# Optimization experiments

Hardware: AMD Instinct MI355X
Metric: run time of the kernel (lower is better)

The kernel has to match this reference:

```python
import jax, jax.numpy as jnp
import numpy as np

B, S, D = 1024, 200, 512
D_FF = 256


def setup_inputs() -> dict:
    key = jax.random.key(0)
    ks = jax.random.split(key, 8)
    s = 0.02  # init scale to keep gates in a sane range
    return {
        "target": jax.random.normal(ks[0], (B, D), jnp.float32),
        "history": jax.random.normal(ks[1], (B, S, D), jnp.float32),
        "W_ih": jax.random.normal(ks[2], (3 * D, D), jnp.float32) * s,
        "W_hh": jax.random.normal(ks[3], (3 * D, D), jnp.float32) * s,
        "b_ih": jnp.zeros((3 * D,), jnp.float32),
        "b_hh": jnp.zeros((3 * D,), jnp.float32),
        "W_fc": jax.random.normal(ks[4], (D_FF, 2 * D), jnp.float32) * s,
        "b_fc": jnp.zeros((D_FF,), jnp.float32),
        "W_sc": jax.random.normal(ks[5], (1, D_FF), jnp.float32) * s,
        "b_sc": jnp.zeros((1,), jnp.float32),
    }


def _gru(history, W_ih, W_hh, b_ih, b_hh):
    # Precompute input-side gate pre-activations for all steps: [B, S, 3D]
    gx = jnp.einsum("bsd,gd->bsg", history, W_ih) + b_ih
    d = history.shape[-1]
    h0 = jnp.zeros((history.shape[0], d), history.dtype)

    def step(h, gx_t):
        gh = h @ W_hh.T + b_hh  # [B, 3D]
        xr, xz, xn = jnp.split(gx_t, 3, axis=-1)
        hr, hz, hn = jnp.split(gh, 3, axis=-1)
        r = jax.nn.sigmoid(xr + hr)
        z = jax.nn.sigmoid(xz + hz)
        n = jnp.tanh(xn + r * hn)
        h_new = (1.0 - z) * n + z * h
        return h_new, h_new

    _, out = jax.lax.scan(step, h0, jnp.swapaxes(gx, 0, 1))  # out: [S, B, D]
    return jnp.swapaxes(out, 0, 1)  # [B, S, D]


def reference(target, history, W_ih, W_hh, b_ih, b_hh, W_fc, b_fc, W_sc, b_sc):
    d = target.shape[-1]
    gru_out = _gru(history, W_ih, W_hh, b_ih, b_hh)  # [B, S, D]

    # concat([gru_out, target]) @ W_fc.T  == gru_out @ Wg.T + target @ Wt.T
    Wg, Wt = W_fc[:, :d], W_fc[:, d:]
    pre = jnp.einsum("bsd,fd->bsf", gru_out, Wg) + (target @ Wt.T)[:, None, :] + b_fc
    hidden = jax.nn.gelu(pre, approximate=False)  # torch F.gelu default is exact erf
    scores = jnp.einsum("bsf,f->bs", hidden, W_sc[0]) + b_sc[0]  # [B, S]
    w = jax.nn.softmax(scores, axis=-1)
    interest = jnp.einsum("bs,bsd->bd", w, gru_out)  # [B, D]
    return jnp.concatenate([interest, target], axis=-1)  # [B, 2D]
```

## Files before the change

kernel.cpp:

```cpp
#include <hip/hip_runtime.h>

typedef __attribute__((ext_vector_type(8))) short short8v;
typedef __attribute__((ext_vector_type(4))) float f32x4;

#define NB 1024
#define NS 200
#define ND 512
#define NG 1536
#define NM 204800
#define NFF 256

#define GRU_P 4
#define GRU_G 64

__device__ __forceinline__ float bf2f(unsigned short u){
  union { unsigned u; float f; } v; v.u = ((unsigned)u) << 16; return v.f;
}
__device__ __forceinline__ unsigned short f2bf(float f){
  union { float f; unsigned u; } v; v.f = f;
  unsigned r = v.u + 0x7fffu + ((v.u >> 16) & 1u);
  return (unsigned short)(r >> 16);
}
__device__ __forceinline__ float sigm(float x){ return 1.f / (1.f + __expf(-x)); }
__device__ __forceinline__ float tanhfast(float x){ return 1.f - 2.f / (1.f + __expf(2.f * x)); }

__global__ void k_prepack(const float* __restrict__ W, unsigned short* __restrict__ out,
                          int ld, int coloff, int ntiles){
  int gid = blockIdx.x * 256 + threadIdx.x;
  if (gid >= ntiles * 1024) return;
  int ntile = gid >> 10; int rem = gid & 1023;
  int kk = rem >> 6; int lane = rem & 63;
  int c = ntile * 16 + (lane & 15);
  int k0 = kk * 32 + (lane >> 4) * 8;
  const float* s = W + (size_t)c * ld + coloff + k0;
  uint4 v;
  v.x = (unsigned)f2bf(s[0]) | ((unsigned)f2bf(s[1]) << 16);
  v.y = (unsigned)f2bf(s[2]) | ((unsigned)f2bf(s[3]) << 16);
  v.z = (unsigned)f2bf(s[4]) | ((unsigned)f2bf(s[5]) << 16);
  v.w = (unsigned)f2bf(s[6]) | ((unsigned)f2bf(s[7]) << 16);
  *(uint4*)(out + (size_t)gid * 8) = v;
}

__global__ void k_tvec(const float* __restrict__ target, const float* __restrict__ Wfc,
                       const float* __restrict__ bfc, float* __restrict__ tvec){
  __shared__ float tg[4][ND];
  int bb = blockIdx.x;
  int tid = threadIdx.x;
  for (int idx = tid; idx < 4 * ND; idx += 256){
    int j = idx >> 9, d = idx & 511;
    tg[j][d] = target[(size_t)(bb * 4 + j) * ND + d];
  }
  __syncthreads();
  const float* wrow = Wfc + (size_t)tid * 1024 + 512;
  float a0 = 0, a1 = 0, a2 = 0, a3 = 0;
  for (int d = 0; d < ND; ++d){
    float wv = wrow[d];
    a0 += tg[0][d] * wv; a1 += tg[1][d] * wv; a2 += tg[2][d] * wv; a3 += tg[3][d] * wv;
  }
  float bias = bfc[tid];
  tvec[(size_t)(bb * 4 + 0) * NFF + tid] = a0 + bias;
  tvec[(size_t)(bb * 4 + 1) * NFF + tid] = a1 + bias;
  tvec[(size_t)(bb * 4 + 2) * NFF + tid] = a2 + bias;
  tvec[(size_t)(bb * 4 + 3) * NFF + tid] = a3 + bias;
}

__global__ __launch_bounds__(256) void k_gemm_gx(const float* __restrict__ Af,
                                                 const unsigned short* __restrict__ Bpk,
                                                 const float* __restrict__ bih,
                                                 unsigned short* __restrict__ gx){
  __shared__ unsigned short As[128 * 64];
  int tid = threadIdx.x; int lane = tid & 63; int wid = tid >> 6;
  int wm = wid >> 1, wn = wid & 1;
  int Nb = blockIdx.x, Mb = blockIdx.y;
  const float* Abase = Af + (size_t)Mb * 128 * ND;
  const short8v* Bp = (const short8v*)Bpk;
  f32x4 acc[4][4];
  #pragma unroll
  for (int i = 0; i < 4; ++i)
    #pragma unroll
    for (int j = 0; j < 4; ++j) acc[i][j] = (f32x4){0.f, 0.f, 0.f, 0.f};

  for (int kc = 0; kc < 8; ++kc){
    __syncthreads();
    #pragma unroll
    for (int pass = 0; pass < 4; ++pass){
      int idx = pass * 256 + tid; int r = idx >> 3, ch = idx & 7;
      const float* src = Abase + (size_t)r * ND + kc * 64 + ch * 8;
      float4 f0 = *(const float4*)src;
      float4 f1 = *(const float4*)(src + 4);
      uint4 v;
      v.x = (unsigned)f2bf(f0.x) | ((unsigned)f2bf(f0.y) << 16);
      v.y = (unsigned)f2bf(f0.z) | ((unsigned)f2bf(f0.w) << 16);
      v.z = (unsigned)f2bf(f1.x) | ((unsigned)f2bf(f1.y) << 16);
      v.w = (unsigned)f2bf(f1.z) | ((unsigned)f2bf(f1.w) << 16);
      *(uint4*)&As[r * 64 + ch * 8] = v;
    }
    __syncthreads();
    #pragma unroll
    for (int i = 0; i < 2; ++i){
      short8v a[4];
      #pragma unroll
      for (int mt = 0; mt < 4; ++mt)
        a[mt] = *(const short8v*)&As[(wm * 64 + mt * 16 + (lane & 15)) * 64 + i * 32 + (lane >> 4) * 8];
      #pragma unroll
      for (int nt = 0; nt < 4; ++nt){
        short8v b = Bp[((size_t)(Nb * 8 + wn * 4 + nt) * 16 + (kc * 2 + i)) * 64 + lane];
        #pragma unroll
        for (int mt = 0; mt < 4; ++mt)
          acc[mt][nt] = __builtin_amdgcn_mfma_f32_16x16x32_bf16(a[mt], b, acc[mt][nt], 0, 0, 0);
      }
    }
  }
  #pragma unroll
  for (int mt = 0; mt < 4; ++mt){
    #pragma unroll
    for (int nt = 0; nt < 4; ++nt){
      int gcol = Nb * 128 + wn * 64 + nt * 16 + (lane & 15);
      float bv = bih[gcol];
      #pragma unroll
      for (int r = 0; r < 4; ++r){
        int grow = Mb * 128 + wm * 64 + mt * 16 + (lane >> 4) * 4 + r;
        gx[(size_t)grow * NG + gcol] = f2bf(acc[mt][nt][r] + bv);
      }
    }
  }
}

__global__ __launch_bounds__(512, 1) void k_gru7(const unsigned short* __restrict__ gx,
                                                 const unsigned short* __restrict__ Wpk,
                                                 const float* __restrict__ bhh,
                                                 unsigned short* __restrict__ gout,
                                                 unsigned long long* __restrict__ hx,
                                                 int* __restrict__ flags){
  __shared__ unsigned short hbuf[2][16 * 512];
  __shared__ unsigned short hstg[16][136];
  int tid = threadIdx.x; int lane = tid & 63; int nh = tid >> 6;
  int bid = blockIdx.x; int g = bid & 63; int s = bid >> 6;
  int colg = lane & 15;
  int rowg = lane >> 4;
  int c_h = s * 128 + nh * 16 + colg;
  int b0 = g * 16;
  int* gfl = flags + g * 32;

  for (int i = tid; i < 16 * 512; i += 512) hbuf[0][i] = 0;

  short8v wf[3][16];
  const short8v* Wp = (const short8v*)Wpk;
  #pragma unroll
  for (int gg = 0; gg < 3; ++gg){
    int ntile = gg * 32 + s * 8 + nh;
    #pragma unroll
    for (int kk = 0; kk < 16; ++kk)
      wf[gg][kk] = Wp[((size_t)ntile * 16 + kk) * 64 + lane];
  }
  float bR = bhh[c_h], bZ = bhh[512 + c_h], bN = bhh[1024 + c_h];
  float hreg[4] = {0.f, 0.f, 0.f, 0.f};

  int wbat = tid >> 5;
  int wc4  = tid & 31;

  unsigned short cxr[4], cxz[4], cxn[4];
  #pragma unroll
  for (int r = 0; r < 4; ++r){
    const unsigned short* gp = gx + ((size_t)(b0 + rowg * 4 + r) * NS + 0) * NG;
    cxr[r] = gp[c_h]; cxz[r] = gp[512 + c_h]; cxn[r] = gp[1024 + c_h];
  }
  __syncthreads();

  #pragma unroll 1
  for (int t = 0; t < NS; ++t){
    int par = t & 1;
    const unsigned short* hr = hbuf[par];
    f32x4 acc0 = (f32x4){0.f,0.f,0.f,0.f}, acc1 = acc0, acc2 = acc0;
    #pragma unroll
    for (int kc = 0; kc < 16; ++kc){
      short8v a = *(const short8v*)&hr[kc * 512 + lane * 8];
      acc0 = __builtin_amdgcn_mfma_f32_16x16x32_bf16(a, wf[0][kc], acc0, 0, 0, 0);
      acc1 = __builtin_amdgcn_mfma_f32_16x16x32_bf16(a, wf[1][kc], acc1, 0, 0, 0);
      acc2 = __builtin_amdgcn_mfma_f32_16x16x32_bf16(a, wf[2][kc], acc2, 0, 0, 0);
    }
    unsigned short hnew[4];
    #pragma unroll
    for (int r = 0; r < 4; ++r){
      float rr = sigm(bf2f(cxr[r]) + acc0[r] + bR);
      float zz = sigm(bf2f(cxz[r]) + acc1[r] + bZ);
      float nn = tanhfast(bf2f(cxn[r]) + rr * (acc2[r] + bN));
      float h = nn + zz * (hreg[r] - nn);
      hreg[r] = h;
      hnew[r] = f2bf(h);
    }

    if (t + 1 < NS){
      unsigned long long* hxp = hx + (size_t)par * (1024 * 128);
      #pragma unroll
      for (int r = 0; r < 4; ++r) hstg[rowg * 4 + r][nh * 16 + colg] = hnew[r];
      __syncthreads();
      {
        unsigned long long v8 = *(const unsigned long long*)&hstg[wbat][wc4 * 4];
        __hip_atomic_store(&hxp[(size_t)(b0 + wbat) * 128 + s * 32 + wc4], v8,
                           __ATOMIC_RELAXED, __HIP_MEMORY_SCOPE_AGENT);
      }
      asm volatile("s_waitcnt vmcnt(0)" ::: "memory");
      if (lane == 0)
        __hip_atomic_store(&gfl[s * 8 + nh], t + 1, __ATOMIC_RELAXED, __HIP_MEMORY_SCOPE_AGENT);
      #pragma unroll
      for (int r = 0; r < 4; ++r)
        gout[((size_t)(b0 + rowg * 4 + r) * NS + t) * ND + c_h] = hnew[r];
      #pragma unroll
      for (int r = 0; r < 4; ++r){
        const unsigned short* gp = gx + ((size_t)(b0 + rowg * 4 + r) * NS + (t + 1)) * NG;
        cxr[r] = gp[c_h]; cxz[r] = gp[512 + c_h]; cxn[r] = gp[1024 + c_h];
      }
      {
        int need = t + 1; int fv;
        do {
          fv = (lane < 32) ? __hip_atomic_load(&gfl[lane], __ATOMIC_RELAXED, __HIP_MEMORY_SCOPE_AGENT) : need;
        } while (!__all(fv >= need));
      }
      unsigned short* hw = hbuf[par ^ 1];
      #pragma unroll
      for (int q = 0; q < 2; ++q){
        int kc = q * 8 + nh;
        size_t base = (size_t)(b0 + (lane & 15)) * 128 + kc * 8 + (lane >> 4) * 2;
        unsigned long long u0 = __hip_atomic_load(&hxp[base],     __ATOMIC_RELAXED, __HIP_MEMORY_SCOPE_AGENT);
        unsigned long long u1 = __hip_atomic_load(&hxp[base + 1], __ATOMIC_RELAXED, __HIP_MEMORY_SCOPE_AGENT);
        unsigned long long tmp[2] = {u0, u1};
        *(uint4*)&hw[kc * 512 + lane * 8] = *(const uint4*)tmp;
      }
      __syncthreads();
    } else {
      #pragma unroll
      for (int r = 0; r < 4; ++r)
        gout[((size_t)(b0 + rowg * 4 + r) * NS + t) * ND + c_h] = hnew[r];
    }
  }
}

__global__ __launch_bounds__(512) void k_gemm_s4(const unsigned short* __restrict__ A,
                                                 const unsigned short* __restrict__ Bpk,
                                                 const float* __restrict__ tvec,
                                                 const float* __restrict__ Wsc,
                                                 const float* __restrict__ bsc,
                                                 float* __restrict__ scores){
  __shared__ unsigned short As[128 * 64];
  __shared__ float spart[4][128];
  int tid = threadIdx.x; int lane = tid & 63; int wid = tid >> 6;
  int wm = wid >> 2, wn = wid & 3;
  int Mb = blockIdx.x;
  const unsigned short* Abase = A + (size_t)Mb * 128 * ND;
  const short8v* Bp = (const short8v*)Bpk;
  f32x4 acc[4][4];
  #pragma unroll
  for (int i = 0; i < 4; ++i)
    #pragma unroll
    for (int j = 0; j < 4; ++j) acc[i][j] = (f32x4){0.f, 0.f, 0.f, 0.f};

  for (int kc = 0; kc < 8; ++kc){
    __syncthreads();
    #pragma unroll
    for (int pass = 0; pass < 2; ++pass){
      int idx = pass * 512 + tid; int r = idx >> 3, ch = idx & 7;
      uint4 v = *(const uint4*)(Abase + (size_t)r * ND + kc * 64 + ch * 8);
      *(uint4*)&As[r * 64 + ch * 8] = v;
    }
    __syncthreads();
    #pragma unroll
    for (int i = 0; i < 2; ++i){
      short8v a[4];
      #pragma unroll
      for (int mt = 0; mt < 4; ++mt)
        a[mt] = *(const short8v*)&As[(wm * 64 + mt * 16 + (lane & 15)) * 64 + i * 32 + (lane >> 4) * 8];
      #pragma unroll
      for (int nt = 0; nt < 4; ++nt){
        short8v b = Bp[((size_t)(wn * 4 + nt) * 16 + (kc * 2 + i)) * 64 + lane];
        #pragma unroll
        for (int mt = 0; mt < 4; ++mt)
          acc[mt][nt] = __builtin_amdgcn_mfma_f32_16x16x32_bf16(a[mt], b, acc[mt][nt], 0, 0, 0);
      }
    }
  }
  #pragma unroll
  for (int mt = 0; mt < 4; ++mt){
    #pragma unroll
    for (int r = 0; r < 4; ++r){
      int rowl = wm * 64 + mt * 16 + (lane >> 4) * 4 + r;
      unsigned grow = (unsigned)(Mb * 128 + rowl);
      unsigned bidx = grow / 200u;
      float rowsum = 0.f;
      #pragma unroll
      for (int nt = 0; nt < 4; ++nt){
        int gcol = wn * 64 + nt * 16 + (lane & 15);
        float pre = acc[mt][nt][r] + tvec[(size_t)bidx * NFF + gcol];
        float g = 0.5f * pre * (1.f + erff(pre * 0.70710678118654752f));
        rowsum += g * Wsc[gcol];
      }
      rowsum += __shfl_xor(rowsum, 1, 64);
      rowsum += __shfl_xor(rowsum, 2, 64);
      rowsum += __shfl_xor(rowsum, 4, 64);
      rowsum += __shfl_xor(rowsum, 8, 64);
      if ((lane & 15) == 0) spart[wn][rowl] = rowsum;
    }
  }
  __syncthreads();
  if (tid < 128){
    float s = spart[0][tid] + spart[1][tid] + spart[2][tid] + spart[3][tid] + bsc[0];
    scores[(size_t)Mb * 128 + tid] = s;
  }
}

__global__ void k_out(const float* __restrict__ scores, const unsigned short* __restrict__ gout,
                      const float* __restrict__ target, float* __restrict__ out){
  int b = blockIdx.x; int tid = threadIdx.x;
  __shared__ float sw[NS];
  __shared__ float red[4];
  float v = (tid < NS) ? scores[(size_t)b * NS + tid] : -3.0e38f;
  float m = v;
  #pragma unroll
  for (int off = 32; off >= 1; off >>= 1) m = fmaxf(m, __shfl_xor(m, off, 64));
  if ((tid & 63) == 0) red[tid >> 6] = m;
  __syncthreads();
  m = fmaxf(fmaxf(red[0], red[1]), fmaxf(red[2], red[3]));
  float e = (tid < NS) ? __expf(v - m) : 0.f;
  if (tid < NS) sw[tid] = e;
  float su = e;
  #pragma unroll
  for (int off = 32; off >= 1; off >>= 1) su += __shfl_xor(su, off, 64);
  __syncthreads();
  if ((tid & 63) == 0) red[tid >> 6] = su;
  __syncthreads();
  float inv = 1.f / (red[0] + red[1] + red[2] + red[3]);
  int d0 = tid * 2;
  float a0 = 0.f, a1 = 0.f;
  const unsigned short* gbase = gout + (size_t)b * NS * ND + d0;
  for (int s = 0; s < NS; ++s){
    unsigned u = *(const unsigned*)(gbase + (size_t)s * ND);
    float wgt = sw[s];
    a0 += wgt * bf2f((unsigned short)(u & 0xffffu));
    a1 += wgt * bf2f((unsigned short)(u >> 16));
  }
  out[(size_t)b * 1024 + d0] = a0 * inv;
  out[(size_t)b * 1024 + d0 + 1] = a1 * inv;
  float2 tv = *(const float2*)(target + (size_t)b * ND + d0);
  out[(size_t)b * 1024 + 512 + d0] = tv.x;
  out[(size_t)b * 1024 + 512 + d0 + 1] = tv.y;
}

extern "C" void kernel_launch(void* const* d_in, const int* in_sizes, int n_in,
                              void* d_out, int out_size, void* d_ws, size_t ws_size,
                              hipStream_t stream) {
  const float* target  = (const float*)d_in[0];
  const float* history = (const float*)d_in[1];
  const float* W_ih    = (const float*)d_in[2];
  const float* W_hh    = (const float*)d_in[3];
  const float* b_ih    = (const float*)d_in[4];
  const float* b_hh    = (const float*)d_in[5];
  const float* W_fc    = (const float*)d_in[6];
  const float* b_fc    = (const float*)d_in[7];
  const float* W_sc    = (const float*)d_in[8];
  const float* b_sc    = (const float*)d_in[9];

  char* ws = (char*)d_ws;
  size_t off = 0;
  unsigned short* gx     = (unsigned short*)(ws + off); off += 629145600ull;
  unsigned short* gout   = (unsigned short*)(ws + off); off += 209715200ull;
  unsigned short* wih_pk = (unsigned short*)(ws + off); off += 1572864ull;
  unsigned short* whh_pk = (unsigned short*)(ws + off); off += 1572864ull;
  unsigned short* wg_pk  = (unsigned short*)(ws + off); off += 262144ull;
  float*          tvec   = (float*)(ws + off);          off += 1048576ull;
  float*          scores = (float*)(ws + off);          off += 819200ull;
  unsigned long long* hx = (unsigned long long*)(ws + off); off += 2097152ull;
  int*            flags  = (int*)(ws + off);             off += 8192ull;
  if (ws_size < off) return;
  float* outp = (float*)d_out;

  (void)hipMemsetAsync(flags, 0, GRU_G * 32 * sizeof(int), stream);
  k_prepack<<<384, 256, 0, stream>>>(W_ih, wih_pk, 512, 0, 96);
  k_prepack<<<384, 256, 0, stream>>>(W_hh, whh_pk, 512, 0, 96);
  k_prepack<<<64, 256, 0, stream>>>(W_fc, wg_pk, 1024, 0, 16);
  k_tvec<<<256, 256, 0, stream>>>(target, W_fc, b_fc, tvec);
  k_gemm_gx<<<dim3(12, 1600), 256, 0, stream>>>(history, wih_pk, b_ih, gx);
  k_gru7<<<256, 512, 0, stream>>>(gx, whh_pk, b_hh, gout, hx, flags);
  k_gemm_s4<<<1600, 512, 0, stream>>>(gout, wg_pk, tvec, W_sc, b_sc, scores);
  k_out<<<1024, 256, 0, stream>>>(scores, gout, target, outp);
}
```

Baseline: 2.041 ms.

## Narrow GRU step sync to per-wave flag pairs and fold r/z hidden bias

The GRU recurrent kernel replaces the block-wide barrier before publishing h with a wave-local LDS wait, since each wave now publishes only its own staged columns. Instead of every wave polling all 32 producer flags, each wave polls two 64-bit flag pairs covering only the k-chunks it consumes, and loads each half as soon as its producers are ready. The r/z parts of b_hh are folded into the gx GEMM bias epilogue, removing two adds per element per step. This cuts the serial per-timestep synchronization latency, but the correctness of the finer-grained dependency tracking is more delicate.

```diff
diff --git a/kernel.cpp b/kernel.cpp
--- a/kernel.cpp
+++ b/kernel.cpp
@@ -67,6 +67,7 @@
 __global__ __launch_bounds__(256) void k_gemm_gx(const float* __restrict__ Af,
                                                  const unsigned short* __restrict__ Bpk,
                                                  const float* __restrict__ bih,
+                                                 const float* __restrict__ bhh,
                                                  unsigned short* __restrict__ gx){
   __shared__ unsigned short As[128 * 64];
   int tid = threadIdx.x; int lane = tid & 63; int wid = tid >> 6;
@@ -116,7 +117,7 @@
     #pragma unroll
     for (int nt = 0; nt < 4; ++nt){
       int gcol = Nb * 128 + wn * 64 + nt * 16 + (lane & 15);
-      float bv = bih[gcol];
+      float bv = bih[gcol] + (gcol < 1024 ? bhh[gcol] : 0.f);
       #pragma unroll
       for (int r = 0; r < 4; ++r){
         int grow = Mb * 128 + wm * 64 + mt * 16 + (lane >> 4) * 4 + r;
@@ -126,7 +127,7 @@
   }
 }
 
-__global__ __launch_bounds__(512, 1) void k_gru7(const unsigned short* __restrict__ gx,
+__global__ __launch_bounds__(512, 1) void k_gru9(const unsigned short* __restrict__ gx,
                                                  const unsigned short* __restrict__ Wpk,
                                                  const float* __restrict__ bhh,
                                                  unsigned short* __restrict__ gout,
@@ -153,11 +154,12 @@
     for (int kk = 0; kk < 16; ++kk)
       wf[gg][kk] = Wp[((size_t)ntile * 16 + kk) * 64 + lane];
   }
-  float bR = bhh[c_h], bZ = bhh[512 + c_h], bN = bhh[1024 + c_h];
+  float bN = bhh[1024 + c_h];
   float hreg[4] = {0.f, 0.f, 0.f, 0.f};
 
-  int wbat = tid >> 5;
-  int wc4  = tid & 31;
+  int wpair = (nh & 3) * 2;
+  const unsigned long long* f1 = (const unsigned long long*)&gfl[(nh >> 2) * 8 + wpair];
+  const unsigned long long* f2 = (const unsigned long long*)&gfl[((nh >> 2) + 2) * 8 + wpair];
 
   unsigned short cxr[4], cxz[4], cxn[4];
   #pragma unroll
@@ -182,8 +184,8 @@
     unsigned short hnew[4];
     #pragma unroll
     for (int r = 0; r < 4; ++r){
-      float rr = sigm(bf2f(cxr[r]) + acc0[r] + bR);
-      float zz = sigm(bf2f(cxz[r]) + acc1[r] + bZ);
+      float rr = sigm(bf2f(cxr[r]) + acc0[r]);
+      float zz = sigm(bf2f(cxz[r]) + acc1[r]);
       float nn = tanhfast(bf2f(cxn[r]) + rr * (acc2[r] + bN));
       float h = nn + zz * (hreg[r] - nn);
       hreg[r] = h;
@@ -194,10 +196,10 @@
       unsigned long long* hxp = hx + (size_t)par * (1024 * 128);
       #pragma unroll
       for (int r = 0; r < 4; ++r) hstg[rowg * 4 + r][nh * 16 + colg] = hnew[r];
-      __syncthreads();
+      asm volatile("s_waitcnt lgkmcnt(0)" ::: "memory");
       {
-        unsigned long long v8 = *(const unsigned long long*)&hstg[wbat][wc4 * 4];
-        __hip_atomic_store(&hxp[(size_t)(b0 + wbat) * 128 + s * 32 + wc4], v8,
+        unsigned long long v8 = *(const unsigned long long*)&hstg[lane & 15][nh * 16 + (lane >> 4) * 4];
+        __hip_atomic_store(&hxp[(size_t)(b0 + (lane & 15)) * 128 + s * 32 + nh * 4 + (lane >> 4)], v8,
                            __ATOMIC_RELAXED, __HIP_MEMORY_SCOPE_AGENT);
       }
       asm volatile("s_waitcnt vmcnt(0)" ::: "memory");
@@ -211,22 +213,25 @@
         const unsigned short* gp = gx + ((size_t)(b0 + rowg * 4 + r) * NS + (t + 1)) * NG;
         cxr[r] = gp[c_h]; cxz[r] = gp[512 + c_h]; cxn[r] = gp[1024 + c_h];
       }
-      {
-        int need = t + 1; int fv;
-        do {
-          fv = (lane < 32) ? __hip_atomic_load(&gfl[lane], __ATOMIC_RELAXED, __HIP_MEMORY_SCOPE_AGENT) : need;
-        } while (!__all(fv >= need));
-      }
+      int need = t + 1;
+      unsigned long long fa;
+      do {
+        fa = __hip_atomic_load(f1, __ATOMIC_RELAXED, __HIP_MEMORY_SCOPE_AGENT);
+      } while ((int)(fa & 0xffffffffu) < need || (int)(fa >> 32) < need);
+      asm volatile("" ::: "memory");
+      size_t base1 = (size_t)(b0 + (lane & 15)) * 128 + nh * 8 + (lane >> 4) * 2;
+      unsigned long long u0 = __hip_atomic_load(&hxp[base1],     __ATOMIC_RELAXED, __HIP_MEMORY_SCOPE_AGENT);
+      unsigned long long u1 = __hip_atomic_load(&hxp[base1 + 1], __ATOMIC_RELAXED, __HIP_MEMORY_SCOPE_AGENT);
+      do {
+        fa = __hip_atomic_load(f2, __ATOMIC_RELAXED, __HIP_MEMORY_SCOPE_AGENT);
+      } while ((int)(fa & 0xffffffffu) < need || (int)(fa >> 32) < need);
+      asm volatile("" ::: "memory");
+      size_t base2 = base1 + 64;
+      unsigned long long u2 = __hip_atomic_load(&hxp[base2],     __ATOMIC_RELAXED, __HIP_MEMORY_SCOPE_AGENT);
+      unsigned long long u3 = __hip_atomic_load(&hxp[base2 + 1], __ATOMIC_RELAXED, __HIP_MEMORY_SCOPE_AGENT);
       unsigned short* hw = hbuf[par ^ 1];
-      #pragma unroll
-      for (int q = 0; q < 2; ++q){
-        int kc = q * 8 + nh;
-        size_t base = (size_t)(b0 + (lane & 15)) * 128 + kc * 8 + (lane >> 4) * 2;
-        unsigned long long u0 = __hip_atomic_load(&hxp[base],     __ATOMIC_RELAXED, __HIP_MEMORY_SCOPE_AGENT);
-        unsigned long long u1 = __hip_atomic_load(&hxp[base + 1], __ATOMIC_RELAXED, __HIP_MEMORY_SCOPE_AGENT);
-        unsigned long long tmp[2] = {u0, u1};
-        *(uint4*)&hw[kc * 512 + lane * 8] = *(const uint4*)tmp;
-      }
+      { unsigned long long tmp[2] = {u0, u1}; *(uint4*)&hw[nh * 512 + lane * 8] = *(const uint4*)tmp; }
+      { unsigned long long tmp[2] = {u2, u3}; *(uint4*)&hw[(nh + 8) * 512 + lane * 8] = *(const uint4*)tmp; }
       __syncthreads();
     } else {
       #pragma unroll
@@ -378,8 +383,8 @@
   k_prepack<<<384, 256, 0, stream>>>(W_hh, whh_pk, 512, 0, 96);
   k_prepack<<<64, 256, 0, stream>>>(W_fc, wg_pk, 1024, 0, 16);
   k_tvec<<<256, 256, 0, stream>>>(target, W_fc, b_fc, tvec);
-  k_gemm_gx<<<dim3(12, 1600), 256, 0, stream>>>(history, wih_pk, b_ih, gx);
-  k_gru7<<<256, 512, 0, stream>>>(gx, whh_pk, b_hh, gout, hx, flags);
+  k_gemm_gx<<<dim3(12, 1600), 256, 0, stream>>>(history, wih_pk, b_ih, b_hh, gx);
+  k_gru9<<<256, 512, 0, stream>>>(gx, whh_pk, b_hh, gout, hx, flags);
   k_gemm_s4<<<1600, 512, 0, stream>>>(gout, wg_pk, tvec, W_sc, b_sc, scores);
   k_out<<<1024, 256, 0, stream>>>(scores, gout, target, outp);
 }
```

Result: slower. 2.352 ms (+15.2%).
